# Kernel tuning notes

Hardware: AMD Instinct MI355X
Metric: run time of the kernel (lower is better)

## Reference

```python
import jax, jax.numpy as jnp
import numpy as np
from math import factorial, sqrt

RS_IN = [(64, 0, 0), (64, 1, 0), (32, 2, 0)]
BATCH = 256


def _w3j(j1, j2, j3, m1, m2, m3):
    # Racah formula for the Wigner 3j symbol (integer l's)
    if m1 + m2 + m3 != 0 or not (abs(j1 - j2) <= j3 <= j1 + j2):
        return 0.0
    if abs(m1) > j1 or abs(m2) > j2 or abs(m3) > j3:
        return 0.0
    f = factorial
    pref = (-1.0) ** (j1 - j2 - m3) * sqrt(
        f(j1 + j2 - j3) * f(j1 - j2 + j3) * f(-j1 + j2 + j3) / f(j1 + j2 + j3 + 1)
        * f(j1 + m1) * f(j1 - m1) * f(j2 + m2) * f(j2 - m2) * f(j3 + m3) * f(j3 - m3))
    kmin = max(0, j2 - j3 - m1, j1 - j3 + m2)
    kmax = min(j1 + j2 - j3, j1 - m1, j2 + m2)
    s = 0.0
    for k in range(kmin, kmax + 1):
        s += (-1.0) ** k / (f(k) * f(j1 + j2 - j3 - k) * f(j1 - m1 - k)
                            * f(j2 + m2 - k) * f(j3 - j2 + m1 + k) * f(j3 - j1 - m2 + k))
    return pref * s


def _q(l):
    # unitary change of basis: complex spherical harmonics -> real basis
    q = np.zeros((2 * l + 1, 2 * l + 1), dtype=complex)
    q[l, l] = 1.0
    for m in range(1, l + 1):
        q[l + m, l + m] = (-1) ** m / sqrt(2)
        q[l + m, l - m] = 1 / sqrt(2)
        q[l - m, l - m] = 1j / sqrt(2)
        q[l - m, l + m] = -1j * (-1) ** m / sqrt(2)
    return q


def _real_w3j(la, lb, lc):
    # real-basis Wigner 3j tensor of shape (2la+1, 2lb+1, 2lc+1), Frobenius norm 1
    Cc = np.zeros((2 * la + 1, 2 * lb + 1, 2 * lc + 1))
    for ma in range(-la, la + 1):
        for mb in range(-lb, lb + 1):
            mc = -(ma + mb)
            if abs(mc) <= lc:
                Cc[la + ma, lb + mb, lc + mc] = _w3j(la, lb, lc, ma, mb, mc)
    T = np.einsum('im,jn,ko,mno->ijk', _q(la), _q(lb), _q(lc), Cc.astype(complex))
    idx = np.argmax(np.abs(T))
    T = T / (T.flat[idx] / abs(T.flat[idx]))  # fix global phase -> real tensor
    assert np.abs(T.imag).max() < 1e-6
    return np.real(T)


def _simplify(Rs):
    out = []
    for mul, l, p in Rs:
        if out and out[-1][1:] == (l, p):
            out[-1] = (out[-1][0] + mul, l, p)
        elif mul > 0:
            out.append((mul, l, p))
    return out


def _build(Rs_in):
    # Replicates e3nn tensor_square(Rs_in, sorted=True) with 'component' normalization,
    # producing the sparse mixing matrix as (row, col_i, col_j, value) with
    # col = col_i * dim_in + col_j  (never materialized densely).
    Rs = _simplify(Rs_in)
    dim_in = sum(m * (2 * l + 1) for m, l, _ in Rs)
    rows, ci, cj, vals, Rs_out = [], [], [], [], []
    index_out = 0
    index_1 = 0
    for a, (mul1, l1, p1) in enumerate(Rs):
        dim1 = mul1 * (2 * l1 + 1)
        # diagonal block: irrep with itself (sym/antisym multiplicity pairs)
        for lo in range(0, 2 * l1 + 1):
            w_all = np.arange(mul1 * mul1)
            u, v = w_all // mul1, w_all % mul1
            mask = (u <= v) if lo % 2 == 0 else (u < v)
            u, v = u[mask], v[mask]
            cnt = u.size
            if cnt == 0:
                continue
            C = _real_w3j(lo, l1, l1) * sqrt(2 * lo + 1)  # component norm
            k, i1, i2 = np.nonzero(C)
            cv = C[k, i1, i2]
            w = np.arange(cnt)
            rows.append((w[:, None] * (2 * lo + 1) + k[None, :]).ravel() + index_out)
            ci.append((u[:, None] * (2 * l1 + 1) + i1[None, :]).ravel() + index_1)
            cj.append((v[:, None] * (2 * l1 + 1) + i2[None, :]).ravel() + index_1)
            vals.append(np.tile(cv, cnt))
            Rs_out.append((cnt, lo, p1 * p1))
            index_out += cnt * (2 * lo + 1)
        index_2 = index_1 + dim1
        # off-diagonal blocks
        for (mul2, l2, p2) in Rs[a + 1:]:
            dim2 = mul2 * (2 * l2 + 1)
            for lo in range(abs(l1 - l2), l1 + l2 + 1):
                C = _real_w3j(lo, l1, l2) * sqrt(2 * lo + 1)
                k, i1, i2 = np.nonzero(C)
                cv = C[k, i1, i2]
                cnt = mul1 * mul2
                w = np.arange(cnt)
                u, v = w // mul2, w % mul2
                rows.append((w[:, None] * (2 * lo + 1) + k[None, :]).ravel() + index_out)
                ci.append((u[:, None] * (2 * l1 + 1) + i1[None, :]).ravel() + index_1)
                cj.append((v[:, None] * (2 * l2 + 1) + i2[None, :]).ravel() + index_2)
                vals.append(np.tile(cv, cnt))
                Rs_out.append((cnt, lo, p1 * p2))
                index_out += cnt * (2 * lo + 1)
            index_2 += dim2
        index_1 += dim1
    Rs_out = _simplify(Rs_out)
    # stable sort of output irreps by (l, p) -> row permutation (sorted=True)
    xs, j = [], 0
    for mul, l, p in Rs_out:
        d = mul * (2 * l + 1)
        xs.append((l, p, mul, j, d))
        j += d
    old2new = np.empty(j, dtype=np.int64)
    i = 0
    for l, p, mul, jj, d in sorted(xs):
        old2new[jj:jj + d] = np.arange(i, i + d)
        i += d
    rows = old2new[np.concatenate(rows)]
    return (rows.astype(np.int32), np.concatenate(ci).astype(np.int32),
            np.concatenate(cj).astype(np.int32),
            np.concatenate(vals).astype(np.float32), int(i), int(dim_in))


_ROWS, _COLI, _COLJ, _VALS, _DIM_OUT, _DIM_IN = _build(RS_IN)


def setup_inputs() -> dict:
    key = jax.random.key(0)
    features = jax.random.normal(key, (BATCH, _DIM_IN), dtype=jnp.float32)
    return {
        'features': features,
        'vals': jnp.asarray(_VALS),
        'rows': jnp.asarray(_ROWS),
        'col_i': jnp.asarray(_COLI),
        'col_j': jnp.asarray(_COLJ),
        'dim_out': _DIM_OUT,
    }


def reference(features, vals, rows, col_i, col_j, dim_out):
    # out[z, r] = sum_e vals[e] * f[z, col_i[e]] * f[z, col_j[e]]  scattered into rows[e]
    f = features.reshape(-1, features.shape[-1])              # (Z, dim_in)
    contrib = vals[None, :] * f[:, col_i] * f[:, col_j]       # (Z, nnz)
    out = jax.ops.segment_sum(contrib.T, rows, num_segments=dim_out)  # (dim_out, Z)
    return out.T.reshape(*features.shape[:-1], -1)
```

## Files before the change

kernel.cpp:

```cpp
#include <hip/hip_runtime.h>

#define BATCH 256
#define ZTILE 16
#define NZT 4
#define PADF 20
#define CAP 16
#define DIN_CAP 416

__global__ __launch_bounds__(256) void prep(
    const float* __restrict__ f, const int* __restrict__ rows,
    int* __restrict__ rstart, int* __restrict__ rend,
    float* __restrict__ fT, int nnz, int dim_in, int nF, int do_transpose)
{
    const int i = blockIdx.x * blockDim.x + threadIdx.x;
    if (i < nnz) {
        const int r = rows[i];
        if (i == 0 || rows[i - 1] != r) rstart[r] = i;
        if (i == nnz - 1 || rows[i + 1] != r) rend[r] = i + 1;
    }
    if (do_transpose && i < nF) {
        const int z = i / dim_in;
        const int c = i - z * dim_in;
        fT[(size_t)c * BATCH + z] = f[i];
    }
}

__device__ __forceinline__ void lds_sync()
{
    asm volatile("s_waitcnt lgkmcnt(0)" ::: "memory");
    __builtin_amdgcn_sched_barrier(0);
    __builtin_amdgcn_s_barrier();
    __builtin_amdgcn_sched_barrier(0);
}

__global__ __launch_bounds__(256) void tsq_main(
    const float* __restrict__ fT, const float* __restrict__ vals,
    const int* __restrict__ ci, const int* __restrict__ cj,
    const int* __restrict__ rstart, const int* __restrict__ rend,
    float* __restrict__ out, int dim_in, int dim_out, int nnz)
{
    __shared__ __align__(16) float fzT[DIN_CAP * PADF];

    const int r = blockIdx.x * blockDim.x + threadIdx.x;
    const bool valid = (r < dim_out);

    int s = 0, e1 = 0;
    if (valid) {
        const int ss = rstart[r];
        const int ee = rend[r];
        if (ss >= 0 && ee >= ss && ee <= nnz) { s = ss; e1 = ee; }
    }
    const int cnt  = e1 - s;
    const int creg = cnt < CAP ? cnt : CAP;

    int pa_[CAP]; int pb_[CAP]; float ev_[CAP];
#pragma unroll
    for (int i = 0; i < CAP; ++i) {
        if (!__any(i < creg)) break;
        if (i < creg) {
            pa_[i] = ci[s + i] * (PADF * 4);
            pb_[i] = cj[s + i] * (PADF * 4);
            ev_[i] = vals[s + i];
        }
    }

    const int zbase = blockIdx.y * (ZTILE * NZT);
    const int nchunk = dim_in * (ZTILE / 4);

    for (int t = 0; t < NZT; ++t) {
        const int z0 = zbase + t * ZTILE;

        for (int i = threadIdx.x; i < nchunk; i += blockDim.x) {
            const int c  = i >> 2;
            const int zq = i & 3;
            const float4 v = *(const float4*)(fT + (size_t)c * BATCH + z0 + zq * 4);
            *(float4*)(fzT + c * PADF + zq * 4) = v;
        }
        lds_sync();

        float4 a0 = {0,0,0,0}, a1 = {0,0,0,0}, a2 = {0,0,0,0}, a3 = {0,0,0,0};
#pragma unroll
        for (int i = 0; i < CAP; ++i) {
            if (!__any(i < creg)) break;
            if (i < creg) {
                const float v = ev_[i];
                const char* ba = (const char*)fzT + pa_[i];
                const char* bb = (const char*)fzT + pb_[i];
                float4 xa, xb;
                xa = *(const float4*)(ba);      xb = *(const float4*)(bb);
                a0.x += v*xa.x*xb.x; a0.y += v*xa.y*xb.y; a0.z += v*xa.z*xb.z; a0.w += v*xa.w*xb.w;
                xa = *(const float4*)(ba + 16); xb = *(const float4*)(bb + 16);
                a1.x += v*xa.x*xb.x; a1.y += v*xa.y*xb.y; a1.z += v*xa.z*xb.z; a1.w += v*xa.w*xb.w;
                xa = *(const float4*)(ba + 32); xb = *(const float4*)(bb + 32);
                a2.x += v*xa.x*xb.x; a2.y += v*xa.y*xb.y; a2.z += v*xa.z*xb.z; a2.w += v*xa.w*xb.w;
                xa = *(const float4*)(ba + 48); xb = *(const float4*)(bb + 48);
                a3.x += v*xa.x*xb.x; a3.y += v*xa.y*xb.y; a3.z += v*xa.z*xb.z; a3.w += v*xa.w*xb.w;
            }
        }
        for (int e = s + CAP; e < e1; ++e) {
            const int a = ci[e], b = cj[e]; const float v = vals[e];
            const float* ba = fzT + a * PADF;
            const float* bb = fzT + b * PADF;
#pragma unroll
            for (int q = 0; q < 4; ++q) {
                const float4 xa = *(const float4*)(ba + q * 4);
                const float4 xb = *(const float4*)(bb + q * 4);
                float4* ac = q == 0 ? &a0 : q == 1 ? &a1 : q == 2 ? &a2 : &a3;
                ac->x += v*xa.x*xb.x; ac->y += v*xa.y*xb.y;
                ac->z += v*xa.z*xb.z; ac->w += v*xa.w*xb.w;
            }
        }

        if (valid) {
            float* o = out + (size_t)z0 * dim_out + r;
            const size_t d = dim_out;
            __builtin_nontemporal_store(a0.x, o);          __builtin_nontemporal_store(a0.y, o + d);
            __builtin_nontemporal_store(a0.z, o + 2*d);    __builtin_nontemporal_store(a0.w, o + 3*d);
            __builtin_nontemporal_store(a1.x, o + 4*d);    __builtin_nontemporal_store(a1.y, o + 5*d);
            __builtin_nontemporal_store(a1.z, o + 6*d);    __builtin_nontemporal_store(a1.w, o + 7*d);
            __builtin_nontemporal_store(a2.x, o + 8*d);    __builtin_nontemporal_store(a2.y, o + 9*d);
            __builtin_nontemporal_store(a2.z, o + 10*d);   __builtin_nontemporal_store(a2.w, o + 11*d);
            __builtin_nontemporal_store(a3.x, o + 12*d);   __builtin_nontemporal_store(a3.y, o + 13*d);
            __builtin_nontemporal_store(a3.z, o + 14*d);   __builtin_nontemporal_store(a3.w, o + 15*d);
        }
        lds_sync();
    }
}

__global__ __launch_bounds__(256) void tsq_fallback(
    const float* __restrict__ f, const float* __restrict__ vals,
    const int* __restrict__ ci, const int* __restrict__ cj,
    const int* __restrict__ rstart, const int* __restrict__ rend,
    float* __restrict__ out, int dim_in, int dim_out, int nnz)
{
    const int r = blockIdx.x * blockDim.x + threadIdx.x;
    if (r >= dim_out) return;
    const int z = blockIdx.y;
    const float* __restrict__ fb = f + (size_t)z * dim_in;
    const int ss = rstart[r];
    const int ee = rend[r];
    float acc = 0.0f;
    if (ss >= 0 && ee > ss && ee <= nnz) {
        for (int e = ss; e < ee; ++e)
            acc += vals[e] * fb[ci[e]] * fb[cj[e]];
    }
    out[(size_t)z * dim_out + r] = acc;
}

extern "C" void kernel_launch(void* const* d_in, const int* in_sizes, int n_in,
                              void* d_out, int out_size, void* d_ws, size_t ws_size,
                              hipStream_t stream)
{
    const float* f    = (const float*)d_in[0];
    const float* vals = (const float*)d_in[1];
    const int*   rows = (const int*)d_in[2];
    const int*   ci   = (const int*)d_in[3];
    const int*   cj   = (const int*)d_in[4];
    float*       out  = (float*)d_out;

    const int nnz     = in_sizes[1];
    const int nF      = in_sizes[0];
    const int dim_in  = nF / BATCH;
    const int dim_out = out_size / BATCH;

    int*   rstart = (int*)d_ws;
    int*   rend   = rstart + dim_out;
    float* fT     = (float*)(rend + dim_out);

    const int use_main = (dim_in <= DIN_CAP) &&
                         (ws_size >= (size_t)(2 * dim_out) * 4 + (size_t)nF * 4);

    const int prep_n = nnz > nF ? nnz : nF;
    prep<<<(prep_n + 255) / 256, 256, 0, stream>>>(f, rows, rstart, rend, fT,
                                                   nnz, dim_in, nF, use_main);

    if (use_main) {
        dim3 grid((dim_out + 255) / 256, BATCH / (ZTILE * NZT));
        tsq_main<<<grid, 256, 0, stream>>>(fT, vals, ci, cj, rstart, rend, out,
                                           dim_in, dim_out, nnz);
    } else {
        dim3 grid((dim_out + 255) / 256, BATCH);
        tsq_fallback<<<grid, 256, 0, stream>>>(f, vals, ci, cj, rstart, rend,
                                               out, dim_in, dim_out, nnz);
    }
}
```

Before: 36.44 us.

## Tile the feature transpose through LDS, halve z-tiles, drop register-cached pair lists

The prep kernel now transposes features in 32x32 tiles staged through padded shared memory, so both the global reads and the writes are coalesced. Row-range computation moves to separate blocks of the same launch. The main kernel halves NZT, which doubles the grid in the batch dimension for more parallelism. It also stops preloading up to 16 (ci, cj, val) entries into registers and reads them from global memory inside a plain loop, which lowers register pressure but adds repeated index loads for each z-tile.

After: 35.79 us. Within noise of the previous version (-1.8%).

```diff
diff --git a/kernel.cpp b/kernel.cpp
--- a/kernel.cpp
+++ b/kernel.cpp
@@ -2,26 +2,43 @@
 
 #define BATCH 256
 #define ZTILE 16
-#define NZT 4
+#define NZT 2
 #define PADF 20
-#define CAP 16
 #define DIN_CAP 416
 
-__global__ __launch_bounds__(256) void prep(
+__global__ __launch_bounds__(256) void prep_t(
     const float* __restrict__ f, const int* __restrict__ rows,
     int* __restrict__ rstart, int* __restrict__ rend,
-    float* __restrict__ fT, int nnz, int dim_in, int nF, int do_transpose)
+    float* __restrict__ fT, int nnz, int dim_in, int TB, int ctiles)
 {
-    const int i = blockIdx.x * blockDim.x + threadIdx.x;
-    if (i < nnz) {
-        const int r = rows[i];
-        if (i == 0 || rows[i - 1] != r) rstart[r] = i;
-        if (i == nnz - 1 || rows[i + 1] != r) rend[r] = i + 1;
-    }
-    if (do_transpose && i < nF) {
-        const int z = i / dim_in;
-        const int c = i - z * dim_in;
-        fT[(size_t)c * BATCH + z] = f[i];
+    const int bx = blockIdx.x;
+    if (bx < TB) {
+        __shared__ float lt[32][33];
+        const int c0 = (bx % ctiles) * 32;
+        const int z0 = (bx / ctiles) * 32;
+        const int ic = threadIdx.x & 31;
+        const int i0 = threadIdx.x >> 5;
+#pragma unroll
+        for (int k = 0; k < 4; ++k) {
+            const int a = i0 + 8 * k;
+            const int c = c0 + ic;
+            lt[a][ic] = (c < dim_in) ? f[(size_t)(z0 + a) * dim_in + c] : 0.0f;
+        }
+        __syncthreads();
+#pragma unroll
+        for (int k = 0; k < 4; ++k) {
+            const int b = i0 + 8 * k;
+            const int c = c0 + b;
+            if (c < dim_in)
+                fT[(size_t)c * BATCH + z0 + ic] = lt[ic][b];
+        }
+    } else {
+        const int e = (bx - TB) * 256 + threadIdx.x;
+        if (e < nnz) {
+            const int r = rows[e];
+            if (e == 0 || rows[e - 1] != r) rstart[r] = e;
+            if (e == nnz - 1 || rows[e + 1] != r) rend[r] = e + 1;
+        }
     }
 }
 
@@ -48,20 +65,7 @@
     if (valid) {
         const int ss = rstart[r];
         const int ee = rend[r];
-        if (ss >= 0 && ee >= ss && ee <= nnz) { s = ss; e1 = ee; }
-    }
-    const int cnt  = e1 - s;
-    const int creg = cnt < CAP ? cnt : CAP;
-
-    int pa_[CAP]; int pb_[CAP]; float ev_[CAP];
-#pragma unroll
-    for (int i = 0; i < CAP; ++i) {
-        if (!__any(i < creg)) break;
-        if (i < creg) {
-            pa_[i] = ci[s + i] * (PADF * 4);
-            pb_[i] = cj[s + i] * (PADF * 4);
-            ev_[i] = vals[s + i];
-        }
+        if (ss >= 0 && ee > ss && ee <= nnz) { s = ss; e1 = ee; }
     }
 
     const int zbase = blockIdx.y * (ZTILE * NZT);
@@ -79,36 +83,21 @@
         lds_sync();
 
         float4 a0 = {0,0,0,0}, a1 = {0,0,0,0}, a2 = {0,0,0,0}, a3 = {0,0,0,0};
-#pragma unroll
-        for (int i = 0; i < CAP; ++i) {
-            if (!__any(i < creg)) break;
-            if (i < creg) {
-                const float v = ev_[i];
-                const char* ba = (const char*)fzT + pa_[i];
-                const char* bb = (const char*)fzT + pb_[i];
-                float4 xa, xb;
-                xa = *(const float4*)(ba);      xb = *(const float4*)(bb);
-                a0.x += v*xa.x*xb.x; a0.y += v*xa.y*xb.y; a0.z += v*xa.z*xb.z; a0.w += v*xa.w*xb.w;
-                xa = *(const float4*)(ba + 16); xb = *(const float4*)(bb + 16);
-                a1.x += v*xa.x*xb.x; a1.y += v*xa.y*xb.y; a1.z += v*xa.z*xb.z; a1.w += v*xa.w*xb.w;
-                xa = *(const float4*)(ba + 32); xb = *(const float4*)(bb + 32);
-                a2.x += v*xa.x*xb.x; a2.y += v*xa.y*xb.y; a2.z += v*xa.z*xb.z; a2.w += v*xa.w*xb.w;
-                xa = *(const float4*)(ba + 48); xb = *(const float4*)(bb + 48);
-                a3.x += v*xa.x*xb.x; a3.y += v*xa.y*xb.y; a3.z += v*xa.z*xb.z; a3.w += v*xa.w*xb.w;
-            }
-        }
-        for (int e = s + CAP; e < e1; ++e) {
-            const int a = ci[e], b = cj[e]; const float v = vals[e];
+        for (int e = s; e < e1; ++e) {
+            const int   a = ci[e];
+            const int   b = cj[e];
+            const float v = vals[e];
             const float* ba = fzT + a * PADF;
             const float* bb = fzT + b * PADF;
-#pragma unroll
-            for (int q = 0; q < 4; ++q) {
-                const float4 xa = *(const float4*)(ba + q * 4);
-                const float4 xb = *(const float4*)(bb + q * 4);
-                float4* ac = q == 0 ? &a0 : q == 1 ? &a1 : q == 2 ? &a2 : &a3;
-                ac->x += v*xa.x*xb.x; ac->y += v*xa.y*xb.y;
-                ac->z += v*xa.z*xb.z; ac->w += v*xa.w*xb.w;
-            }
+            float4 xa, xb;
+            xa = *(const float4*)(ba);      xb = *(const float4*)(bb);
+            a0.x += v*xa.x*xb.x; a0.y += v*xa.y*xb.y; a0.z += v*xa.z*xb.z; a0.w += v*xa.w*xb.w;
+            xa = *(const float4*)(ba + 4);  xb = *(const float4*)(bb + 4);
+            a1.x += v*xa.x*xb.x; a1.y += v*xa.y*xb.y; a1.z += v*xa.z*xb.z; a1.w += v*xa.w*xb.w;
+            xa = *(const float4*)(ba + 8);  xb = *(const float4*)(bb + 8);
+            a2.x += v*xa.x*xb.x; a2.y += v*xa.y*xb.y; a2.z += v*xa.z*xb.z; a2.w += v*xa.w*xb.w;
+            xa = *(const float4*)(ba + 12); xb = *(const float4*)(bb + 12);
+            a3.x += v*xa.x*xb.x; a3.y += v*xa.y*xb.y; a3.z += v*xa.z*xb.z; a3.w += v*xa.w*xb.w;
         }
 
         if (valid) {
@@ -170,9 +159,11 @@
     const int use_main = (dim_in <= DIN_CAP) &&
                          (ws_size >= (size_t)(2 * dim_out) * 4 + (size_t)nF * 4);
 
-    const int prep_n = nnz > nF ? nnz : nF;
-    prep<<<(prep_n + 255) / 256, 256, 0, stream>>>(f, rows, rstart, rend, fT,
-                                                   nnz, dim_in, nF, use_main);
+    const int ctiles = (dim_in + 31) / 32;
+    const int TB = use_main ? ctiles * (BATCH / 32) : 0;
+    const int NB = (nnz + 255) / 256;
+    prep_t<<<TB + NB, 256, 0, stream>>>(f, rows, rstart, rend, fT,
+                                        nnz, dim_in, TB, ctiles);
 
     if (use_main) {
         dim3 grid((dim_out + 255) / 256, BATCH / (ZTILE * NZT));
```
